# Performance work log

Measured on AMD Instinct MI355X. Metric: run time of the kernel, lower is better.

Reference implementation:

```python
import jax, jax.numpy as jnp
import numpy as np

IN_DIM = 256
HIDDEN = 512
MEM = 256
IN_LEN = 4096
THETA = 4096.0
BATCH = 32


def _expm(M):
    # scaling-and-squaring with Taylor series (float64)
    nrm = max(np.linalg.norm(M, 1), 1e-30)
    s = max(0, int(np.ceil(np.log2(nrm))) + 1)
    A = M / (2.0 ** s)
    d = M.shape[0]
    E = np.eye(d)
    term = np.eye(d)
    for k in range(1, 30):
        term = term @ A / k
        E = E + term
    for _ in range(s):
        E = E @ E
    return E


def _gen_AB(memory_size, theta):
    Q = np.arange(memory_size, dtype=np.float64).reshape(-1, 1)
    R = (2 * Q + 1) / theta
    i, j = np.meshgrid(Q, Q, indexing='ij')
    A = np.where(i < j, -1.0, (-1.0) ** (i - j + 1)) * R
    B = (-1.0) ** Q * R  # [mem, 1]
    # ZOH discretization with dt=1: expm of augmented [[A,B],[0,0]]
    d = memory_size
    em = np.zeros((d + 1, d + 1))
    em[:d, :d] = A
    em[:d, d:] = B
    ed = _expm(em)
    Ad = ed[:d, :d]
    Bd = ed[:d, d:]
    return Ad, Bd


def _impulse(memory_size, in_len, theta):
    Ad, Bd = _gen_AB(memory_size, theta)
    H = np.empty((memory_size, in_len), dtype=np.float64)
    v = Bd.copy()  # [mem, 1]
    for t in range(in_len):
        H[:, t] = v[:, 0]
        v = Ad @ v
    return H.astype(np.float32)


def setup_inputs() -> dict:
    key = jax.random.key(0)
    kx, ku, kh = jax.random.split(key, 3)
    x = jax.random.normal(kx, (BATCH, IN_LEN, IN_DIM), dtype=jnp.float32)
    W_u = jax.random.normal(ku, (1, IN_DIM), dtype=jnp.float32)
    W_h = jax.random.normal(kh, (HIDDEN, MEM + IN_DIM), dtype=jnp.float32)
    H = jnp.asarray(_impulse(MEM, IN_LEN, THETA))  # [mem, in_len]
    return {"x": x, "W_u": W_u, "W_h": W_h, "H": H}


def reference(x, W_u, W_h, H):
    batch, n, _ = x.shape
    # encode: u = relu(x @ W_u^T)  -> [B, n, 1]
    u = jax.nn.relu(jnp.einsum('bni,oi->bno', x, W_u))
    # FFT long convolution with impulse response H
    u_fft = jnp.fft.rfft(u.transpose(0, 2, 1), n=2 * n, axis=-1)  # [B,1,n+1]
    H_fft = jnp.fft.rfft(H, n=2 * n, axis=-1)                      # [mem,n+1]
    m = jnp.fft.irfft(u_fft * H_fft[None], n=2 * n, axis=-1)       # [B,mem,2n]
    m = m[:, :, :n].transpose(0, 2, 1)                             # [B,n,mem]
    # output head: h = relu([m, x] @ W_h^T)
    input_h = jnp.concatenate((m, x), axis=-1)                     # [B,n,mem+in_dim]
    h = jax.nn.relu(jnp.einsum('bnc,oc->bno', input_h, W_h))       # [B,n,hidden]
    h_n = h[:, -1, :]
    return (h, h_n)
```

## Files before the change

### kernel.cpp

```cpp
#include <hip/hip_runtime.h>
#include <hip/hip_bf16.h>
#include <math.h>


#define BATCH 32
#define T     4096
#define IND   256
#define HID   512
#define MEM   256
#define FFT_N 8192
#define FFT_LOG 13
#define BT    131072

typedef __attribute__((ext_vector_type(8))) short short8;
typedef __attribute__((ext_vector_type(8))) _Float16 half8;
typedef __attribute__((ext_vector_type(4))) float f32x4;

__device__ inline short f2bf(float f) {
    unsigned u = __float_as_uint(f);
    unsigned r = (u + 0x7FFFu + ((u >> 16) & 1u)) >> 16;
    return (short)r;
}
__device__ inline unsigned pk2h(float a, float b) {
    union { _Float16 h[2]; unsigned u; } v;
    v.h[0] = (_Float16)a; v.h[1] = (_Float16)b;
    return v.u;
}
__device__ __forceinline__ void gl_lds16(const void* g, void* l) {
    __builtin_amdgcn_global_load_lds((const __attribute__((address_space(1))) unsigned*)g,
                                     (__attribute__((address_space(3))) unsigned*)l, 16, 0, 0);
}

__global__ __launch_bounds__(256) void relu_u_kernel(const float* __restrict__ x,
                                                     const float* __restrict__ Wu,
                                                     float* __restrict__ u,
                                                     _Float16* __restrict__ xh) {
    int wave = threadIdx.x >> 6, lane = threadIdx.x & 63;
    int r = blockIdx.x * 4 + wave;
    const float4 xv = *(const float4*)(x + (size_t)r * IND + lane * 4);
    const float4 wv = *(const float4*)(Wu + lane * 4);
    union { _Float16 h[4]; uint2 u2; } hv;
    hv.h[0] = (_Float16)xv.x; hv.h[1] = (_Float16)xv.y;
    hv.h[2] = (_Float16)xv.z; hv.h[3] = (_Float16)xv.w;
    *(uint2*)(xh + (size_t)r * IND + lane * 4) = hv.u2;
    float acc = xv.x * wv.x + xv.y * wv.y + xv.z * wv.z + xv.w * wv.w;
    for (int off = 32; off; off >>= 1) acc += __shfl_down(acc, off);
    if (lane == 0) u[r] = fmaxf(acc, 0.f);
}
__global__ __launch_bounds__(256) void relu_u_only_kernel(const float* __restrict__ x,
                                                          const float* __restrict__ Wu,
                                                          float* __restrict__ u) {
    int wave = threadIdx.x >> 6, lane = threadIdx.x & 63;
    int r = blockIdx.x * 4 + wave;
    const float4 xv = *(const float4*)(x + (size_t)r * IND + lane * 4);
    const float4 wv = *(const float4*)(Wu + lane * 4);
    float acc = xv.x * wv.x + xv.y * wv.y + xv.z * wv.z + xv.w * wv.w;
    for (int off = 32; off; off >>= 1) acc += __shfl_down(acc, off);
    if (lane == 0) u[r] = fmaxf(acc, 0.f);
}

__global__ __launch_bounds__(256) void wh_pack_kernel(const float* __restrict__ Wh,
                                                      _Float16* __restrict__ whfT) {
    int i = blockIdx.x * 256 + threadIdx.x;
    int col = i >> 7;
    int kq  = (i & 127) << 2;
    float4 v = *(const float4*)(Wh + (size_t)col * HID + kq);
    _Float16* d = whfT + (size_t)(kq >> 3) * (HID * 8) + (size_t)col * 8 + (kq & 7);
    d[0] = (_Float16)v.x; d[1] = (_Float16)v.y;
    d[2] = (_Float16)v.z; d[3] = (_Float16)v.w;
}

__device__ void fft_fwd_r4(float* re, float* im) {
    __syncthreads();
    {
        const float fm = -(float)M_PI / 4096.f;
#pragma unroll
        for (int s = 0; s < 8; ++s) {
            int k = threadIdx.x + s * 512;
            float sn, cs; __sincosf(fm * (float)k, &sn, &cs);
            float ar = re[k], ai = im[k], br = re[k + 4096], bi = im[k + 4096];
            re[k] = ar + br; im[k] = ai + bi;
            float dr = ar - br, di = ai - bi;
            re[k + 4096] = cs * dr - sn * di;
            im[k + 4096] = cs * di + sn * dr;
        }
        __syncthreads();
    }
    for (int st = 10; st >= 0; st -= 2) {
        int q = 1 << st;
        float fm = -(float)M_PI / (float)(2 * q);
#pragma unroll
        for (int s = 0; s < 4; ++s) {
            int k = threadIdx.x + s * 512;
            int j = k & (q - 1);
            int i0 = ((k >> st) << (st + 2)) + j;
            float ar = re[i0],         ai = im[i0];
            float br = re[i0 + q],     bi = im[i0 + q];
            float cr = re[i0 + 2 * q], ci = im[i0 + 2 * q];
            float dr = re[i0 + 3 * q], di = im[i0 + 3 * q];
            float t0r = ar + cr, t0i = ai + ci;
            float t1r = ar - cr, t1i = ai - ci;
            float t2r = br + dr, t2i = bi + di;
            float t3r = bi - di, t3i = dr - br;
            float sn, cs; __sincosf(fm * (float)j, &sn, &cs);
            float w2r = cs * cs - sn * sn, w2i = 2.f * cs * sn;
            float w3r = w2r * cs - w2i * sn, w3i = w2r * sn + w2i * cs;
            re[i0] = t0r + t2r;               im[i0] = t0i + t2i;
            float er = t0r - t2r, ei = t0i - t2i;
            re[i0 + q] = er * w2r - ei * w2i; im[i0 + q] = er * w2i + ei * w2r;
            float fr = t1r + t3r, fi = t1i + t3i;
            re[i0 + 2 * q] = fr * cs - fi * sn; im[i0 + 2 * q] = fr * sn + fi * cs;
            float gr = t1r - t3r, gi = t1i - t3i;
            re[i0 + 3 * q] = gr * w3r - gi * w3i; im[i0 + 3 * q] = gr * w3i + gi * w3r;
        }
        __syncthreads();
    }
}
__device__ void fft_inv_r4(float* re, float* im) {
    __syncthreads();
    for (int st = 0; st <= 10; st += 2) {
        int q = 1 << st;
        float fm = (float)M_PI / (float)(2 * q);
#pragma unroll
        for (int s = 0; s < 4; ++s) {
            int k = threadIdx.x + s * 512;
            int j = k & (q - 1);
            int i0 = ((k >> st) << (st + 2)) + j;
            float Ar = re[i0],         Ai = im[i0];
            float Br = re[i0 + q],     Bi = im[i0 + q];
            float Cr = re[i0 + 2 * q], Ci = im[i0 + 2 * q];
            float Dr = re[i0 + 3 * q], Di = im[i0 + 3 * q];
            float sn, cs; __sincosf(fm * (float)j, &sn, &cs);
            float w2r = cs * cs - sn * sn, w2i = 2.f * cs * sn;
            float w3r = w2r * cs - w2i * sn, w3i = w2r * sn + w2i * cs;
            float bpr = Br * w2r - Bi * w2i, bpi = Br * w2i + Bi * w2r;
            float cpr = Cr * cs - Ci * sn,   cpi = Cr * sn + Ci * cs;
            float dpr = Dr * w3r - Di * w3i, dpi = Dr * w3i + Di * w3r;
            float t0r = Ar + bpr, t0i = Ai + bpi;
            float t2r = Ar - bpr, t2i = Ai - bpi;
            float t1r = cpr + dpr, t1i = cpi + dpi;
            float t3r = cpr - dpr, t3i = cpi - dpi;
            re[i0]         = t0r + t1r; im[i0]         = t0i + t1i;
            re[i0 + 2 * q] = t0r - t1r; im[i0 + 2 * q] = t0i - t1i;
            re[i0 + q]     = t2r - t3i; im[i0 + q]     = t2i + t3r;
            re[i0 + 3 * q] = t2r + t3i; im[i0 + 3 * q] = t2i - t3r;
        }
        __syncthreads();
    }
    {
        const float fm = (float)M_PI / 4096.f;
#pragma unroll
        for (int s = 0; s < 8; ++s) {
            int k = threadIdx.x + s * 512;
            float sn, cs; __sincosf(fm * (float)k, &sn, &cs);
            float br = re[k + 4096], bi = im[k + 4096];
            float tr = cs * br - sn * bi, ti = cs * bi + sn * br;
            float ar = re[k], ai = im[k];
            re[k] = ar + tr;        im[k] = ai + ti;
            re[k + 4096] = ar - tr; im[k + 4096] = ai - ti;
        }
        __syncthreads();
    }
}

__global__ __launch_bounds__(512) void fwd_all_kernel(const float* __restrict__ u,
                                                      const float* __restrict__ H,
                                                      float2* __restrict__ Uf,
                                                      float2* __restrict__ Hf) {
    __shared__ float re[FFT_N];
    __shared__ float im[FFT_N];
    int r = blockIdx.x;
    const float* src = (r < BATCH) ? (u + (size_t)r * T) : (H + (size_t)(r - BATCH) * T);
    float2* dst = (r < BATCH) ? (Uf + (size_t)r * FFT_N) : (Hf + (size_t)(r - BATCH) * FFT_N);
    for (int i = threadIdx.x; i < FFT_N; i += 512) {
        re[i] = (i < T) ? src[i] : 0.f;
        im[i] = 0.f;
    }
    fft_fwd_r4(re, im);
    for (int i = threadIdx.x; i < FFT_N; i += 512) dst[i] = make_float2(re[i], im[i]);
}

__global__ __launch_bounds__(512) void conv_m_kernel(const float2* __restrict__ Uf,
                                                     const float2* __restrict__ Hf,
                                                     _Float16* __restrict__ m2) {
    int qb = blockIdx.x;
    int b  = blockIdx.y;
    __shared__ float re[FFT_N];
    __shared__ float im[FFT_N];
    const float2* Ub = Uf + (size_t)b * FFT_N;
    const float inv = 1.0f / (float)FFT_N;
    unsigned p0[8], p1[8], p2[8], p3[8];

#define DO_FF(FF, PK)                                                          \
    {                                                                          \
        const float2* Ha = Hf + (size_t)(qb * 8 + 2 * (FF)) * FFT_N;           \
        const float2* Hb = Ha + FFT_N;                                         \
        for (int f = threadIdx.x; f < FFT_N; f += 512) {                       \
            float2 uv = Ub[f], h0 = Ha[f], h1 = Hb[f];                         \
            float gr = h0.x - h1.y, gi = h0.y + h1.x;           \
            re[f] = uv.x * gr - uv.y * gi;                                     \
            im[f] = uv.x * gi + uv.y * gr;                                     \
        }                                                                      \
        fft_inv_r4(re, im);                                                    \
        _Pragma("unroll")                                                      \
        for (int it = 0; it < 8; ++it) {                                       \
            int tt = threadIdx.x + it * 512;                                   \
            PK[it] = pk2h(re[tt] * inv, im[tt] * inv);                         \
        }                                                                      \
    }

    DO_FF(0, p0)
    DO_FF(1, p1)
    DO_FF(2, p2)
    DO_FF(3, p3)
#undef DO_FF

    _Float16* dst = m2 + ((size_t)qb * BT + (size_t)b * T) * 8;
#pragma unroll
    for (int it = 0; it < 8; ++it) {
        int tt = threadIdx.x + it * 512;
        uint4 w;
        w.x = p0[it]; w.y = p1[it]; w.z = p2[it]; w.w = p3[it];
        *(uint4*)(dst + (size_t)tt * 8) = w;
    }
}

__global__ __launch_bounds__(256) void h_gemm_kernel(const _Float16* __restrict__ xh,
                                                     const _Float16* __restrict__ whfT,
                                                     const _Float16* __restrict__ m2,
                                                     float* __restrict__ out) {
    __shared__ __align__(16) _Float16 As[8][128][8];
    __shared__ __align__(16) _Float16 Bs[8][128][8];
    int bn = blockIdx.x;
    int bm = blockIdx.y;
    int t = threadIdx.x;
    int wv = t >> 6, lane = t & 63;
    int wm = (wv & 1) * 64, wn = (wv >> 1) * 64;
    int ln = lane & 15, kg = lane >> 4;

    f32x4 acc[4][4] = {};
#pragma unroll
    for (int ks = 0; ks < 8; ++ks) {
        int kc = ks * 64;
        __syncthreads();
#pragma unroll
        for (int q = 0; q < 8; ++q) {
            int c = wv * 8 + q;
            int g = (c & 15) >> 1;
            int rg = c & 1;
            int row = rg * 64 + lane;
            if (c < 16) {
                const void* src;
                if (kc < MEM)
                    src = m2 + ((size_t)(kc / 8 + g) * BT + (size_t)bm * 128 + row) * 8;
                else
                    src = xh + (size_t)(bm * 128 + row) * IND + (kc - MEM) + g * 8;
                gl_lds16(src, &As[g][rg * 64][0]);
            } else {
                const void* src = whfT + (size_t)(kc / 8 + g) * (HID * 8)
                                       + (size_t)(bn * 128 + row) * 8;
                gl_lds16(src, &Bs[g][rg * 64][0]);
            }
        }
        __syncthreads();
        half8 af[2][4], bf[2][4];
#pragma unroll
        for (int kk = 0; kk < 2; ++kk) {
#pragma unroll
            for (int i = 0; i < 4; ++i)
                af[kk][i] = *(const half8*)&As[kk * 4 + kg][wm + i * 16 + ln][0];
#pragma unroll
            for (int j = 0; j < 4; ++j)
                bf[kk][j] = *(const half8*)&Bs[kk * 4 + kg][wn + j * 16 + ln][0];
        }
#pragma unroll
        for (int kk = 0; kk < 2; ++kk)
#pragma unroll
            for (int i = 0; i < 4; ++i)
#pragma unroll
                for (int j = 0; j < 4; ++j)
                    acc[i][j] = __builtin_amdgcn_mfma_f32_16x16x32_f16(af[kk][i], bf[kk][j],
                                                                       acc[i][j], 0, 0, 0);
    }
#pragma unroll
    for (int i = 0; i < 4; ++i) {
#pragma unroll
        for (int j = 0; j < 4; ++j) {
#pragma unroll
            for (int r = 0; r < 4; ++r) {
                int row = bm * 128 + wm + i * 16 + kg * 4 + r;
                int col = bn * 128 + wn + j * 16 + ln;
                float v = fmaxf(acc[i][j][r], 0.f);
                out[(size_t)row * HID + col] = v;
                if ((row & (T - 1)) == (T - 1))
                    out[(size_t)BATCH * T * HID + (size_t)(row >> 12) * HID + col] = v;
            }
        }
    }
}

__device__ void fft_dif_fwd(float* re, float* im) {
    __syncthreads();
    for (int st = FFT_LOG; st >= 1; --st) {
        int half = 1 << (st - 1);
        float fm = -(float)M_PI / (float)half;
        for (int k = threadIdx.x; k < FFT_N / 2; k += 512) {
            int j  = k & (half - 1);
            int i1 = ((k >> (st - 1)) << st) + j;
            int i2 = i1 + half;
            float sn, cs;
            __sincosf(fm * (float)j, &sn, &cs);
            float ar = re[i1], ai = im[i1];
            float br = re[i2], bi = im[i2];
            re[i1] = ar + br; im[i1] = ai + bi;
            float dr = ar - br, di = ai - bi;
            re[i2] = cs * dr - sn * di;
            im[i2] = cs * di + sn * dr;
        }
        __syncthreads();
    }
}
__device__ void fft_dit_inv(float* re, float* im) {
    __syncthreads();
    for (int st = 1; st <= FFT_LOG; ++st) {
        int half = 1 << (st - 1);
        float fm = (float)M_PI / (float)half;
        for (int k = threadIdx.x; k < FFT_N / 2; k += 512) {
            int j  = k & (half - 1);
            int i1 = ((k >> (st - 1)) << st) + j;
            int i2 = i1 + half;
            float sn, cs;
            __sincosf(fm * (float)j, &sn, &cs);
            float br = re[i2], bi = im[i2];
            float tr = cs * br - sn * bi;
            float ti = cs * bi + sn * br;
            float ar = re[i1], ai = im[i1];
            re[i1] = ar + tr; im[i1] = ai + ti;
            re[i2] = ar - tr; im[i2] = ai - ti;
        }
        __syncthreads();
    }
}
__global__ __launch_bounds__(512) void fft_u_kernel(const float* __restrict__ u,
                                                    float2* __restrict__ Uf) {
    int b = blockIdx.x;
    __shared__ float re[FFT_N];
    __shared__ float im[FFT_N];
    for (int i = threadIdx.x; i < FFT_N; i += 512) {
        re[i] = i < T ? u[(size_t)b * T + i] : 0.f;
        im[i] = 0.f;
    }
    fft_dif_fwd(re, im);
    for (int i = threadIdx.x; i < FFT_N; i += 512)
        Uf[(size_t)b * FFT_N + i] = make_float2(re[i], im[i]);
}
__global__ __launch_bounds__(512) void g_fft_kernel(const float* __restrict__ Wh,
                                                    const float* __restrict__ H,
                                                    float2* __restrict__ Gf) {
    int o = blockIdx.x;
    __shared__ float re[FFT_N];
    __shared__ float im[FFT_N];
    const float* wrow = Wh + (size_t)o * HID;
    float acc[8];
#pragma unroll
    for (int d = 0; d < 8; ++d) acc[d] = 0.f;
    for (int q = 0; q < 256; ++q) {
        float w = wrow[q];
        const float* hrow = H + (size_t)q * T;
#pragma unroll
        for (int d = 0; d < 8; ++d)
            acc[d] = fmaf(w, hrow[threadIdx.x + d * 512], acc[d]);
    }
#pragma unroll
    for (int d = 0; d < 8; ++d) {
        re[threadIdx.x + d * 512] = acc[d];
        im[threadIdx.x + d * 512] = 0.f;
    }
    for (int i = T + threadIdx.x; i < FFT_N; i += 512) { re[i] = 0.f; im[i] = 0.f; }
    fft_dif_fwd(re, im);
    for (int i = threadIdx.x; i < FFT_N; i += 512)
        Gf[(size_t)o * FFT_N + i] = make_float2(re[i], im[i]);
}
__global__ __launch_bounds__(256) void xw_gemm_kernel(const float* __restrict__ x,
                                                      const float* __restrict__ Wh,
                                                      float* __restrict__ out) {
    __shared__ __align__(16) short Asl[4][128][8];
    __shared__ __align__(16) short Bsl[4][128][8];
    int bn = blockIdx.x;
    int bm = blockIdx.y;
    int t = threadIdx.x;
    int wv = t >> 6, lane = t & 63;
    int wm = (wv & 1) * 64, wn = (wv >> 1) * 64;
    int ln = lane & 15, kg = lane >> 4;
    f32x4 acc[4][4] = {};
    int mrow = t >> 1, khalf = t & 1;
    for (int kc = 0; kc < IND; kc += 32) {
        {
            const float* xr = x + ((size_t)(bm * 128 + mrow)) * IND + kc + khalf * 16;
            float4 v0 = *(const float4*)(xr + 0);
            float4 v1 = *(const float4*)(xr + 4);
            float4 v2 = *(const float4*)(xr + 8);
            float4 v3 = *(const float4*)(xr + 12);
            short8 s0 = { f2bf(v0.x), f2bf(v0.y), f2bf(v0.z), f2bf(v0.w),
                          f2bf(v1.x), f2bf(v1.y), f2bf(v1.z), f2bf(v1.w) };
            short8 s1 = { f2bf(v2.x), f2bf(v2.y), f2bf(v2.z), f2bf(v2.w),
                          f2bf(v3.x), f2bf(v3.y), f2bf(v3.z), f2bf(v3.w) };
            const float* wr = Wh + ((size_t)(bn * 128 + mrow)) * HID + 256 + kc + khalf * 16;
            float4 w0 = *(const float4*)(wr + 0);
            float4 w1 = *(const float4*)(wr + 4);
            float4 w2 = *(const float4*)(wr + 8);
            float4 w3 = *(const float4*)(wr + 12);
            short8 b0 = { f2bf(w0.x), f2bf(w0.y), f2bf(w0.z), f2bf(w0.w),
                          f2bf(w1.x), f2bf(w1.y), f2bf(w1.z), f2bf(w1.w) };
            short8 b1 = { f2bf(w2.x), f2bf(w2.y), f2bf(w2.z), f2bf(w2.w),
                          f2bf(w3.x), f2bf(w3.y), f2bf(w3.z), f2bf(w3.w) };
            __syncthreads();
            *(short8*)&Asl[khalf * 2 + 0][mrow][0] = s0;
            *(short8*)&Asl[khalf * 2 + 1][mrow][0] = s1;
            *(short8*)&Bsl[khalf * 2 + 0][mrow][0] = b0;
            *(short8*)&Bsl[khalf * 2 + 1][mrow][0] = b1;
            __syncthreads();
        }
        short8 af[4], bf[4];
#pragma unroll
        for (int i = 0; i < 4; ++i) af[i] = *(short8*)&Asl[kg][wm + i * 16 + ln][0];
#pragma unroll
        for (int j = 0; j < 4; ++j) bf[j] = *(short8*)&Bsl[kg][wn + j * 16 + ln][0];
#pragma unroll
        for (int i = 0; i < 4; ++i)
#pragma unroll
            for (int j = 0; j < 4; ++j)
                acc[i][j] = __builtin_amdgcn_mfma_f32_16x16x32_bf16(af[i], bf[j], acc[i][j], 0, 0, 0);
    }
#pragma unroll
    for (int i = 0; i < 4; ++i) {
#pragma unroll
        for (int j = 0; j < 4; ++j) {
#pragma unroll
            for (int r = 0; r < 4; ++r) {
                int row = bm * 128 + wm + i * 16 + (lane >> 4) * 4 + r;
                int col = bn * 128 + wn + j * 16 + (lane & 15);
                out[(size_t)row * HID + col] = acc[i][j][r];
            }
        }
    }
}
__global__ __launch_bounds__(512) void conv_apply_kernel(const float2* __restrict__ Uf,
                                                         const float2* __restrict__ Gf,
                                                         float* __restrict__ out) {
    int p = blockIdx.x;
    int b = blockIdx.y;
    __shared__ float re[FFT_N];
    __shared__ float im[FFT_N];
    const float2* Ub = Uf + (size_t)b * FFT_N;
    const float2* G0 = Gf + (size_t)(2 * p) * FFT_N;
    const float2* G1 = Gf + (size_t)(2 * p + 1) * FFT_N;
    for (int f = threadIdx.x; f < FFT_N; f += 512) {
        float2 uv = Ub[f], g0 = G0[f], g1 = G1[f];
        float gr = g0.x - g1.y, gi = g0.y + g1.x;
        re[f] = uv.x * gr - uv.y * gi;
        im[f] = uv.x * gi + uv.y * gr;
    }
    fft_dit_inv(re, im);
    const float inv = 1.0f / (float)FFT_N;
    for (int t = threadIdx.x; t < T; t += 512) {
        size_t idx = ((size_t)(b * T + t)) * HID + 2 * p;
        float2 xw = *(const float2*)(out + idx);
        float v0 = fmaxf(fmaf(re[t], inv, xw.x), 0.f);
        float v1 = fmaxf(fmaf(im[t], inv, xw.y), 0.f);
        *(float2*)(out + idx) = make_float2(v0, v1);
        if (t == T - 1) {
            size_t hn = (size_t)BATCH * T * HID + (size_t)b * HID + 2 * p;
            *(float2*)(out + hn) = make_float2(v0, v1);
        }
    }
}

extern "C" void kernel_launch(void* const* d_in, const int* in_sizes, int n_in,
                              void* d_out, int out_size, void* d_ws, size_t ws_size,
                              hipStream_t stream) {
    const float* x  = (const float*)d_in[0];
    const float* Wu = (const float*)d_in[1];
    const float* Wh = (const float*)d_in[2];
    const float* H  = (const float*)d_in[3];
    float* out = (float*)d_out;

    char* ws = (char*)d_ws;

    const size_t off_u   = 0;
    const size_t off_xh  = off_u  + 524288;
    const size_t off_whf = off_xh + 67108864;
    const size_t off_U   = off_whf + 524288;
    const size_t off_Hf  = off_U  + 2097152;
    const size_t off_m2  = off_Hf + 16777216;
    const size_t need    = off_m2 + (size_t)MEM * BT * 2;

    if (ws_size >= need) {
        float*     ws_u    = (float*)(ws + off_u);
        _Float16*  ws_xh   = (_Float16*)(ws + off_xh);
        _Float16*  ws_whfT = (_Float16*)(ws + off_whf);
        float2*    ws_U    = (float2*)(ws + off_U);
        float2*    ws_Hf   = (float2*)(ws + off_Hf);
        _Float16*  ws_m2   = (_Float16*)(ws + off_m2);

        wh_pack_kernel<<<HID * HID / 4 / 256, 256, 0, stream>>>(Wh, ws_whfT);
        relu_u_kernel<<<BT / 4, 256, 0, stream>>>(x, Wu, ws_u, ws_xh);
        fwd_all_kernel<<<BATCH + MEM, 512, 0, stream>>>(ws_u, H, ws_U, ws_Hf);
        conv_m_kernel<<<dim3(MEM / 8, BATCH), 512, 0, stream>>>(ws_U, ws_Hf, ws_m2);
        h_gemm_kernel<<<dim3(HID / 128, BT / 128), 256, 0, stream>>>(ws_xh, ws_whfT, ws_m2, out);
    } else {
        float*  ws_u = (float*)ws;
        float2* ws_U = (float2*)(ws + 524288);
        float2* ws_G = (float2*)(ws + 524288 + 2097152);
        relu_u_only_kernel<<<BT / 4, 256, 0, stream>>>(x, Wu, ws_u);
        fft_u_kernel<<<BATCH, 512, 0, stream>>>(ws_u, ws_U);
        g_fft_kernel<<<HID, 512, 0, stream>>>(Wh, H, ws_G);
        xw_gemm_kernel<<<dim3(HID / 128, BATCH * T / 128), 256, 0, stream>>>(x, Wh, out);
        conv_apply_kernel<<<dim3(HID / 2, BATCH), 512, 0, stream>>>(ws_U, ws_G, out);
    }
}
```

Measured before the change: 668.8 us.

## Precompute FFT twiddles and do first/last radix-4 stages in registers

Adds a small kernel that writes forward and inverse twiddle tables to workspace, so the FFT stages load twiddles instead of calling sincos per butterfly. The forward FFT fuses the first radix-2 stage into the global load, and both FFTs run their small-stride stages (q=1,4) in registers on 16 contiguous elements per thread. This removes two LDS passes and their barriers per FFT. The inverse FFT also fuses its final radix-2 stage with the fp16 packing. The cost is an extra launch, table reads from global or cache, and higher register pressure.

Measured after the change: 757.5 us. 13.3% more time.

```diff
diff --git a/kernel.cpp b/kernel.cpp
--- a/kernel.cpp
+++ b/kernel.cpp
@@ -29,6 +29,36 @@
 __device__ __forceinline__ void gl_lds16(const void* g, void* l) {
     __builtin_amdgcn_global_load_lds((const __attribute__((address_space(1))) unsigned*)g,
                                      (__attribute__((address_space(3))) unsigned*)l, 16, 0, 0);
+}
+
+__global__ __launch_bounds__(512) void twiddle_kernel(float2* __restrict__ t4f,
+                                                      float2* __restrict__ t2f,
+                                                      float2* __restrict__ t4i,
+                                                      float2* __restrict__ t2i) {
+    int i = blockIdx.x * 512 + threadIdx.x;
+    if (i < 4096) {
+        float a = ((float)M_PI / 4096.f) * (float)i;
+        float sn, cs; __sincosf(a, &sn, &cs);
+        t2i[i] = make_float2(cs, sn);
+        t2f[i] = make_float2(cs, -sn);
+    } else if (i < 4096 + 1360) {
+        int e = i - 4096;
+        int q, j;
+        if (e < 16)       { q = 16;   j = e; }
+        else if (e < 80)  { q = 64;   j = e - 16; }
+        else if (e < 336) { q = 256;  j = e - 80; }
+        else              { q = 1024; j = e - 336; }
+        float a = ((float)M_PI / (float)(2 * q)) * (float)j;
+        float sn, cs; __sincosf(a, &sn, &cs);
+        float w2r = cs * cs - sn * sn, w2i = 2.f * cs * sn;
+        float w3r = w2r * cs - w2i * sn, w3i = w2r * sn + w2i * cs;
+        t4i[e * 3 + 0] = make_float2(cs, sn);
+        t4i[e * 3 + 1] = make_float2(w2r, w2i);
+        t4i[e * 3 + 2] = make_float2(w3r, w3i);
+        t4f[e * 3 + 0] = make_float2(cs, -sn);
+        t4f[e * 3 + 1] = make_float2(w2r, -w2i);
+        t4f[e * 3 + 2] = make_float2(w3r, -w3i);
+    }
 }
 
 __global__ __launch_bounds__(256) void relu_u_kernel(const float* __restrict__ x,
@@ -70,30 +100,53 @@
     d[2] = (_Float16)v.z; d[3] = (_Float16)v.w;
 }
 
-__device__ void fft_fwd_r4(float* re, float* im) {
+__global__ __launch_bounds__(512) void fwd_all_kernel(const float* __restrict__ u,
+                                                      const float* __restrict__ H,
+                                                      const float2* __restrict__ t4f,
+                                                      const float2* __restrict__ t2f,
+                                                      float2* __restrict__ Uf,
+                                                      float2* __restrict__ Hf) {
+    __shared__ float re[FFT_N];
+    __shared__ float im[FFT_N];
+    int r = blockIdx.x;
+    int n = threadIdx.x;
+    const float* src = (r < BATCH) ? (u + (size_t)r * T) : (H + (size_t)(r - BATCH) * T);
+    float2* dst = (r < BATCH) ? (Uf + (size_t)r * FFT_N) : (Hf + (size_t)(r - BATCH) * FFT_N);
+
+    {
+        float4 s0 = *(const float4*)(src + 8 * n);
+        float4 s1 = *(const float4*)(src + 8 * n + 4);
+        float2 w8[8];
+        *(float4*)&w8[0] = *(const float4*)(t2f + 8 * n);
+        *(float4*)&w8[2] = *(const float4*)(t2f + 8 * n + 2);
+        *(float4*)&w8[4] = *(const float4*)(t2f + 8 * n + 4);
+        *(float4*)&w8[6] = *(const float4*)(t2f + 8 * n + 6);
+        *(float4*)&re[8 * n]     = s0;
+        *(float4*)&re[8 * n + 4] = s1;
+        float4 z = make_float4(0.f, 0.f, 0.f, 0.f);
+        *(float4*)&im[8 * n]     = z;
+        *(float4*)&im[8 * n + 4] = z;
+        float4 ru0 = make_float4(w8[0].x * s0.x, w8[1].x * s0.y, w8[2].x * s0.z, w8[3].x * s0.w);
+        float4 ru1 = make_float4(w8[4].x * s1.x, w8[5].x * s1.y, w8[6].x * s1.z, w8[7].x * s1.w);
+        float4 iu0 = make_float4(w8[0].y * s0.x, w8[1].y * s0.y, w8[2].y * s0.z, w8[3].y * s0.w);
+        float4 iu1 = make_float4(w8[4].y * s1.x, w8[5].y * s1.y, w8[6].y * s1.z, w8[7].y * s1.w);
+        *(float4*)&re[8 * n + 4096]     = ru0;
+        *(float4*)&re[8 * n + 4096 + 4] = ru1;
+        *(float4*)&im[8 * n + 4096]     = iu0;
+        *(float4*)&im[8 * n + 4096 + 4] = iu1;
+    }
     __syncthreads();
-    {
-        const float fm = -(float)M_PI / 4096.f;
-#pragma unroll
-        for (int s = 0; s < 8; ++s) {
-            int k = threadIdx.x + s * 512;
-            float sn, cs; __sincosf(fm * (float)k, &sn, &cs);
-            float ar = re[k], ai = im[k], br = re[k + 4096], bi = im[k + 4096];
-            re[k] = ar + br; im[k] = ai + bi;
-            float dr = ar - br, di = ai - bi;
-            re[k + 4096] = cs * dr - sn * di;
-            im[k + 4096] = cs * di + sn * dr;
-        }
-        __syncthreads();
-    }
-    for (int st = 10; st >= 0; st -= 2) {
+#pragma unroll
+    for (int st = 10; st >= 4; st -= 2) {
         int q = 1 << st;
-        float fm = -(float)M_PI / (float)(2 * q);
+        int toff = (st == 4) ? 0 : (st == 6) ? 16 : (st == 8) ? 80 : 336;
 #pragma unroll
         for (int s = 0; s < 4; ++s) {
-            int k = threadIdx.x + s * 512;
+            int k = n + s * 512;
             int j = k & (q - 1);
             int i0 = ((k >> st) << (st + 2)) + j;
+            const float2* tw = t4f + (size_t)(toff + j) * 3;
+            float2 W1 = tw[0], W2 = tw[1], W3 = tw[2];
             float ar = re[i0],         ai = im[i0];
             float br = re[i0 + q],     bi = im[i0 + q];
             float cr = re[i0 + 2 * q], ci = im[i0 + 2 * q];
@@ -102,126 +155,175 @@
             float t1r = ar - cr, t1i = ai - ci;
             float t2r = br + dr, t2i = bi + di;
             float t3r = bi - di, t3i = dr - br;
-            float sn, cs; __sincosf(fm * (float)j, &sn, &cs);
+            re[i0] = t0r + t2r;               im[i0] = t0i + t2i;
+            float er = t0r - t2r, ei = t0i - t2i;
+            re[i0 + q] = er * W2.x - ei * W2.y;     im[i0 + q] = er * W2.y + ei * W2.x;
+            float fr = t1r + t3r, fi = t1i + t3i;
+            re[i0 + 2 * q] = fr * W1.x - fi * W1.y; im[i0 + 2 * q] = fr * W1.y + fi * W1.x;
+            float gr = t1r - t3r, gi = t1i - t3i;
+            re[i0 + 3 * q] = gr * W3.x - gi * W3.y; im[i0 + 3 * q] = gr * W3.y + gi * W3.x;
+        }
+        __syncthreads();
+    }
+    {
+        float pr[16], pi[16];
+#pragma unroll
+        for (int s4 = 0; s4 < 4; ++s4) {
+            *(float4*)&pr[4 * s4] = *(float4*)&re[16 * n + 4 * s4];
+            *(float4*)&pi[4 * s4] = *(float4*)&im[16 * n + 4 * s4];
+        }
+#pragma unroll
+        for (int j = 0; j < 4; ++j) {
+            float sn, cs; __sincosf((-(float)M_PI / 8.f) * (float)j, &sn, &cs);
             float w2r = cs * cs - sn * sn, w2i = 2.f * cs * sn;
             float w3r = w2r * cs - w2i * sn, w3i = w2r * sn + w2i * cs;
-            re[i0] = t0r + t2r;               im[i0] = t0i + t2i;
+            float ar = pr[j], ai = pi[j], br = pr[j + 4], bi = pi[j + 4];
+            float cr = pr[j + 8], ci = pi[j + 8], dr = pr[j + 12], di = pi[j + 12];
+            float t0r = ar + cr, t0i = ai + ci;
+            float t1r = ar - cr, t1i = ai - ci;
+            float t2r = br + dr, t2i = bi + di;
+            float t3r = bi - di, t3i = dr - br;
+            pr[j] = t0r + t2r; pi[j] = t0i + t2i;
             float er = t0r - t2r, ei = t0i - t2i;
-            re[i0 + q] = er * w2r - ei * w2i; im[i0 + q] = er * w2i + ei * w2r;
+            pr[j + 4] = er * w2r - ei * w2i;  pi[j + 4] = er * w2i + ei * w2r;
             float fr = t1r + t3r, fi = t1i + t3i;
-            re[i0 + 2 * q] = fr * cs - fi * sn; im[i0 + 2 * q] = fr * sn + fi * cs;
+            pr[j + 8] = fr * cs - fi * sn;    pi[j + 8] = fr * sn + fi * cs;
             float gr = t1r - t3r, gi = t1i - t3i;
-            re[i0 + 3 * q] = gr * w3r - gi * w3i; im[i0 + 3 * q] = gr * w3i + gi * w3r;
-        }
-        __syncthreads();
-    }
-}
-__device__ void fft_inv_r4(float* re, float* im) {
-    __syncthreads();
-    for (int st = 0; st <= 10; st += 2) {
-        int q = 1 << st;
-        float fm = (float)M_PI / (float)(2 * q);
-#pragma unroll
-        for (int s = 0; s < 4; ++s) {
-            int k = threadIdx.x + s * 512;
-            int j = k & (q - 1);
-            int i0 = ((k >> st) << (st + 2)) + j;
-            float Ar = re[i0],         Ai = im[i0];
-            float Br = re[i0 + q],     Bi = im[i0 + q];
-            float Cr = re[i0 + 2 * q], Ci = im[i0 + 2 * q];
-            float Dr = re[i0 + 3 * q], Di = im[i0 + 3 * q];
-            float sn, cs; __sincosf(fm * (float)j, &sn, &cs);
-            float w2r = cs * cs - sn * sn, w2i = 2.f * cs * sn;
-            float w3r = w2r * cs - w2i * sn, w3i = w2r * sn + w2i * cs;
-            float bpr = Br * w2r - Bi * w2i, bpi = Br * w2i + Bi * w2r;
-            float cpr = Cr * cs - Ci * sn,   cpi = Cr * sn + Ci * cs;
-            float dpr = Dr * w3r - Di * w3i, dpi = Dr * w3i + Di * w3r;
-            float t0r = Ar + bpr, t0i = Ai + bpi;
-            float t2r = Ar - bpr, t2i = Ai - bpi;
-            float t1r = cpr + dpr, t1i = cpi + dpi;
-            float t3r = cpr - dpr, t3i = cpi - dpi;
-            re[i0]         = t0r + t1r; im[i0]         = t0i + t1i;
-            re[i0 + 2 * q] = t0r - t1r; im[i0 + 2 * q] = t0i - t1i;
-            re[i0 + q]     = t2r - t3i; im[i0 + q]     = t2i + t3r;
-            re[i0 + 3 * q] = t2r + t3i; im[i0 + 3 * q] = t2i - t3r;
-        }
-        __syncthreads();
-    }
-    {
-        const float fm = (float)M_PI / 4096.f;
-#pragma unroll
-        for (int s = 0; s < 8; ++s) {
-            int k = threadIdx.x + s * 512;
-            float sn, cs; __sincosf(fm * (float)k, &sn, &cs);
-            float br = re[k + 4096], bi = im[k + 4096];
-            float tr = cs * br - sn * bi, ti = cs * bi + sn * br;
-            float ar = re[k], ai = im[k];
-            re[k] = ar + tr;        im[k] = ai + ti;
-            re[k + 4096] = ar - tr; im[k + 4096] = ai - ti;
-        }
-        __syncthreads();
-    }
-}
-
-__global__ __launch_bounds__(512) void fwd_all_kernel(const float* __restrict__ u,
-                                                      const float* __restrict__ H,
-                                                      float2* __restrict__ Uf,
-                                                      float2* __restrict__ Hf) {
-    __shared__ float re[FFT_N];
-    __shared__ float im[FFT_N];
-    int r = blockIdx.x;
-    const float* src = (r < BATCH) ? (u + (size_t)r * T) : (H + (size_t)(r - BATCH) * T);
-    float2* dst = (r < BATCH) ? (Uf + (size_t)r * FFT_N) : (Hf + (size_t)(r - BATCH) * FFT_N);
-    for (int i = threadIdx.x; i < FFT_N; i += 512) {
-        re[i] = (i < T) ? src[i] : 0.f;
-        im[i] = 0.f;
-    }
-    fft_fwd_r4(re, im);
-    for (int i = threadIdx.x; i < FFT_N; i += 512) dst[i] = make_float2(re[i], im[i]);
+            pr[j + 12] = gr * w3r - gi * w3i; pi[j + 12] = gr * w3i + gi * w3r;
+        }
+#pragma unroll
+        for (int g = 0; g < 4; ++g) {
+            float ar = pr[4 * g], ai = pi[4 * g], br = pr[4 * g + 1], bi = pi[4 * g + 1];
+            float cr = pr[4 * g + 2], ci = pi[4 * g + 2], dr = pr[4 * g + 3], di = pi[4 * g + 3];
+            float t0r = ar + cr, t0i = ai + ci;
+            float t1r = ar - cr, t1i = ai - ci;
+            float t2r = br + dr, t2i = bi + di;
+            float t3r = bi - di, t3i = dr - br;
+            pr[4 * g]     = t0r + t2r; pi[4 * g]     = t0i + t2i;
+            pr[4 * g + 1] = t0r - t2r; pi[4 * g + 1] = t0i - t2i;
+            pr[4 * g + 2] = t1r + t3r; pi[4 * g + 2] = t1i + t3i;
+            pr[4 * g + 3] = t1r - t3r; pi[4 * g + 3] = t1i - t3i;
+        }
+#pragma unroll
+        for (int e = 0; e < 8; ++e) {
+            float4 o = make_float4(pr[2 * e], pi[2 * e], pr[2 * e + 1], pi[2 * e + 1]);
+            *(float4*)&dst[16 * n + 2 * e] = o;
+        }
+    }
 }
 
 __global__ __launch_bounds__(512) void conv_m_kernel(const float2* __restrict__ Uf,
                                                      const float2* __restrict__ Hf,
+                                                     const float2* __restrict__ t4i,
+                                                     const float2* __restrict__ t2i,
                                                      _Float16* __restrict__ m2) {
     int qb = blockIdx.x;
     int b  = blockIdx.y;
+    int n  = threadIdx.x;
     __shared__ float re[FFT_N];
     __shared__ float im[FFT_N];
     const float2* Ub = Uf + (size_t)b * FFT_N;
     const float inv = 1.0f / (float)FFT_N;
-    unsigned p0[8], p1[8], p2[8], p3[8];
-
-#define DO_FF(FF, PK)                                                          \
-    {                                                                          \
-        const float2* Ha = Hf + (size_t)(qb * 8 + 2 * (FF)) * FFT_N;           \
-        const float2* Hb = Ha + FFT_N;                                         \
-        for (int f = threadIdx.x; f < FFT_N; f += 512) {                       \
-            float2 uv = Ub[f], h0 = Ha[f], h1 = Hb[f];                         \
-            float gr = h0.x - h1.y, gi = h0.y + h1.x;           \
-            re[f] = uv.x * gr - uv.y * gi;                                     \
-            im[f] = uv.x * gi + uv.y * gr;                                     \
-        }                                                                      \
-        fft_inv_r4(re, im);                                                    \
-        _Pragma("unroll")                                                      \
-        for (int it = 0; it < 8; ++it) {                                       \
-            int tt = threadIdx.x + it * 512;                                   \
-            PK[it] = pk2h(re[tt] * inv, im[tt] * inv);                         \
-        }                                                                      \
-    }
-
-    DO_FF(0, p0)
-    DO_FF(1, p1)
-    DO_FF(2, p2)
-    DO_FF(3, p3)
-#undef DO_FF
+    unsigned pk0[8], pk1[8], pk2[8], pk3[8];
+
+#define CONV_FF(FF, PK)                                                          \
+    {                                                                            \
+        const float2* Ha = Hf + (size_t)(qb * 8 + 2 * (FF)) * FFT_N;             \
+        const float2* Hb = Ha + FFT_N;                                           \
+        float pr[16], pi[16];                                                    \
+        _Pragma("unroll")                                                        \
+        for (int e = 0; e < 16; ++e) {                                           \
+            int f = 16 * n + e;                                                  \
+            float2 uv = Ub[f], h0 = Ha[f], h1 = Hb[f];                           \
+            float gr = h0.x - h1.y, gi = h0.y + h1.x;                            \
+            pr[e] = uv.x * gr - uv.y * gi;                                       \
+            pi[e] = uv.x * gi + uv.y * gr;                                       \
+        }                                                                        \
+        _Pragma("unroll")                             \
+        for (int g = 0; g < 4; ++g) {                                            \
+            float Ar = pr[4*g], Ai = pi[4*g], Br = pr[4*g+1], Bi = pi[4*g+1];    \
+            float Cr = pr[4*g+2], Ci = pi[4*g+2], Dr = pr[4*g+3], Di = pi[4*g+3];\
+            float t0r = Ar+Br, t0i = Ai+Bi, t2r = Ar-Br, t2i = Ai-Bi;            \
+            float t1r = Cr+Dr, t1i = Ci+Di, t3r = Cr-Dr, t3i = Ci-Di;            \
+            pr[4*g]   = t0r+t1r; pi[4*g]   = t0i+t1i;                            \
+            pr[4*g+2] = t0r-t1r; pi[4*g+2] = t0i-t1i;                            \
+            pr[4*g+1] = t2r-t3i; pi[4*g+1] = t2i+t3r;                            \
+            pr[4*g+3] = t2r+t3i; pi[4*g+3] = t2i-t3r;                            \
+        }                                                                        \
+        _Pragma("unroll")                                           \
+        for (int j = 0; j < 4; ++j) {                                            \
+            float sn, cs; __sincosf(((float)M_PI / 8.f) * (float)j, &sn, &cs);   \
+            float w2r = cs*cs - sn*sn, w2i = 2.f*cs*sn;                          \
+            float w3r = w2r*cs - w2i*sn, w3i = w2r*sn + w2i*cs;                  \
+            float Ar = pr[j], Ai = pi[j], Br = pr[j+4], Bi = pi[j+4];            \
+            float Cr = pr[j+8], Ci = pi[j+8], Dr = pr[j+12], Di = pi[j+12];      \
+            float bpr = Br*w2r - Bi*w2i, bpi = Br*w2i + Bi*w2r;                  \
+            float cpr = Cr*cs - Ci*sn,   cpi = Cr*sn + Ci*cs;                    \
+            float dpr = Dr*w3r - Di*w3i, dpi = Dr*w3i + Di*w3r;                  \
+            float t0r = Ar+bpr, t0i = Ai+bpi, t2r = Ar-bpr, t2i = Ai-bpi;        \
+            float t1r = cpr+dpr, t1i = cpi+dpi, t3r = cpr-dpr, t3i = cpi-dpi;    \
+            pr[j]    = t0r+t1r; pi[j]    = t0i+t1i;                              \
+            pr[j+8]  = t0r-t1r; pi[j+8]  = t0i-t1i;                              \
+            pr[j+4]  = t2r-t3i; pi[j+4]  = t2i+t3r;                              \
+            pr[j+12] = t2r+t3i; pi[j+12] = t2i-t3r;                              \
+        }                                                                        \
+        if ((FF) > 0) __syncthreads();              \
+        _Pragma("unroll")                                                        \
+        for (int s4 = 0; s4 < 4; ++s4) {                                         \
+            *(float4*)&re[16*n + 4*s4] = *(float4*)&pr[4*s4];                    \
+            *(float4*)&im[16*n + 4*s4] = *(float4*)&pi[4*s4];                    \
+        }                                                                        \
+        __syncthreads();                                                         \
+        _Pragma("unroll")                       \
+        for (int st = 4; st <= 10; st += 2) {                                    \
+            int q = 1 << st;                                                     \
+            int toff = (st == 4) ? 0 : (st == 6) ? 16 : (st == 8) ? 80 : 336;    \
+            _Pragma("unroll")                                                    \
+            for (int s = 0; s < 4; ++s) {                                        \
+                int k = n + s * 512;                                             \
+                int j = k & (q - 1);                                             \
+                int i0 = ((k >> st) << (st + 2)) + j;                            \
+                const float2* tw = t4i + (size_t)(toff + j) * 3;                 \
+                float2 W1 = tw[0], W2 = tw[1], W3 = tw[2];                       \
+                float Ar = re[i0],       Ai = im[i0];                            \
+                float Br = re[i0+q],     Bi = im[i0+q];                          \
+                float Cr = re[i0+2*q],   Ci = im[i0+2*q];                        \
+                float Dr = re[i0+3*q],   Di = im[i0+3*q];                        \
+                float bpr = Br*W2.x - Bi*W2.y, bpi = Br*W2.y + Bi*W2.x;          \
+                float cpr = Cr*W1.x - Ci*W1.y, cpi = Cr*W1.y + Ci*W1.x;          \
+                float dpr = Dr*W3.x - Di*W3.y, dpi = Dr*W3.y + Di*W3.x;          \
+                float t0r = Ar+bpr, t0i = Ai+bpi, t2r = Ar-bpr, t2i = Ai-bpi;    \
+                float t1r = cpr+dpr, t1i = cpi+dpi, t3r = cpr-dpr, t3i = cpi-dpi;\
+                re[i0]       = t0r+t1r; im[i0]       = t0i+t1i;                  \
+                re[i0+2*q]   = t0r-t1r; im[i0+2*q]   = t0i-t1i;                  \
+                re[i0+q]     = t2r-t3i; im[i0+q]     = t2i+t3r;                  \
+                re[i0+3*q]   = t2r+t3i; im[i0+3*q]   = t2i-t3r;                  \
+            }                                                                    \
+            __syncthreads();                                                     \
+        }                                                                        \
+        _Pragma("unroll")  \
+        for (int s = 0; s < 8; ++s) {                                            \
+            int k = n + 512 * s;                                                 \
+            float2 W = t2i[k];                                                   \
+            float br = re[k + 4096], bi = im[k + 4096];                          \
+            float tr = W.x * br - W.y * bi, ti = W.x * bi + W.y * br;            \
+            PK[s] = pk2h((re[k] + tr) * inv, (im[k] + ti) * inv);                \
+        }                                                                        \
+    }
+
+    CONV_FF(0, pk0)
+    CONV_FF(1, pk1)
+    CONV_FF(2, pk2)
+    CONV_FF(3, pk3)
+#undef CONV_FF
 
     _Float16* dst = m2 + ((size_t)qb * BT + (size_t)b * T) * 8;
 #pragma unroll
-    for (int it = 0; it < 8; ++it) {
-        int tt = threadIdx.x + it * 512;
-        uint4 w;
-        w.x = p0[it]; w.y = p1[it]; w.z = p2[it]; w.w = p3[it];
-        *(uint4*)(dst + (size_t)tt * 8) = w;
+    for (int s = 0; s < 8; ++s) {
+        int tt = n + 512 * s;
+        uint4 w4;
+        w4.x = pk0[s]; w4.y = pk1[s]; w4.z = pk2[s]; w4.w = pk3[s];
+        *(uint4*)(dst + (size_t)tt * 8) = w4;
     }
 }
 
@@ -488,7 +590,11 @@
     char* ws = (char*)d_ws;
 
     const size_t off_u   = 0;
-    const size_t off_xh  = off_u  + 524288;
+    const size_t off_t4i = 524288;
+    const size_t off_t2i = off_t4i + 32768;
+    const size_t off_t4f = off_t2i + 32768;
+    const size_t off_t2f = off_t4f + 32768;
+    const size_t off_xh  = off_t2f + 32768;
     const size_t off_whf = off_xh + 67108864;
     const size_t off_U   = off_whf + 524288;
     const size_t off_Hf  = off_U  + 2097152;
@@ -497,16 +603,21 @@
 
     if (ws_size >= need) {
         float*     ws_u    = (float*)(ws + off_u);
+        float2*    ws_t4i  = (float2*)(ws + off_t4i);
+        float2*    ws_t2i  = (float2*)(ws + off_t2i);
+        float2*    ws_t4f  = (float2*)(ws + off_t4f);
+        float2*    ws_t2f  = (float2*)(ws + off_t2f);
         _Float16*  ws_xh   = (_Float16*)(ws + off_xh);
         _Float16*  ws_whfT = (_Float16*)(ws + off_whf);
         float2*    ws_U    = (float2*)(ws + off_U);
         float2*    ws_Hf   = (float2*)(ws + off_Hf);
         _Float16*  ws_m2   = (_Float16*)(ws + off_m2);
 
+        twiddle_kernel<<<11, 512, 0, stream>>>(ws_t4f, ws_t2f, ws_t4i, ws_t2i);
         wh_pack_kernel<<<HID * HID / 4 / 256, 256, 0, stream>>>(Wh, ws_whfT);
         relu_u_kernel<<<BT / 4, 256, 0, stream>>>(x, Wu, ws_u, ws_xh);
-        fwd_all_kernel<<<BATCH + MEM, 512, 0, stream>>>(ws_u, H, ws_U, ws_Hf);
-        conv_m_kernel<<<dim3(MEM / 8, BATCH), 512, 0, stream>>>(ws_U, ws_Hf, ws_m2);
+        fwd_all_kernel<<<BATCH + MEM, 512, 0, stream>>>(ws_u, H, ws_t4f, ws_t2f, ws_U, ws_Hf);
+        conv_m_kernel<<<dim3(MEM / 8, BATCH), 512, 0, stream>>>(ws_U, ws_Hf, ws_t4i, ws_t2i, ws_m2);
         h_gemm_kernel<<<dim3(HID / 128, BT / 128), 256, 0, stream>>>(ws_xh, ws_whfT, ws_m2, out);
     } else {
         float*  ws_u = (float*)ws;
```
